# Performance work log

Hardware: AMD Instinct MI355X
Metric: run time of the kernel (lower is better)

Reference implementation:

```python
import jax, jax.numpy as jnp
import numpy as np

NX = 2048
NY = 2048
PML = 40
DT = 0.0005
DX = 10.0


def setup_inputs() -> dict:
    key = jax.random.key(0)
    k1, k2, k3, k4 = jax.random.split(key, 4)
    pad = 2 * PML
    p1 = jax.random.normal(k1, (NX + pad, NY + pad), dtype=jnp.float32)
    p2 = jax.random.normal(k2, (NX + pad, NY + pad), dtype=jnp.float32)
    varray = jax.random.uniform(k3, (NX, NY), dtype=jnp.float32)
    source_function = jax.random.normal(k4, (500,), dtype=jnp.float32)
    return {
        "p1": p1,
        "p2": p2,
        "varray": varray,
        "source_function": source_function,
        "x_s": 1024,
        "y_s": 1024,
        "t": 100,
    }


def reference(p1, p2, varray, source_function, x_s, y_s, t):
    # Extend velocity model with edge-replicated PML padding (same math as the
    # torch extend_with_pml with its 9 slice assignments).
    pml_varray = jnp.pad(varray, PML, mode="edge")
    alpha = pml_varray ** 2 * (DT ** 2)
    inv_dx2 = 1.0 / (DX * DX)
    # Second-order centered differences via shifted slices.
    dpdx = (p2[:, 9:-7] - 2.0 * p2[:, 8:-8] + p2[:, 7:-9]) * inv_dx2  # [Np, Np-16]
    dpdy = (p2[9:-7, :] - 2.0 * p2[8:-8, :] + p2[7:-9, :]) * inv_dx2  # [Np-16, Np]
    rhs = (
        2.0 * p2[8:-8, 8:-8]
        - p1[8:-8, 8:-8]
        + alpha[8:-8, 8:-8] * (dpdx[8:-8, :] + dpdy[:, 8:-8])
    )
    p = jnp.zeros_like(p1).at[8:-8, 8:-8].set(rhs)
    # Point-source injection at the (offset) source location.
    p = p.at[x_s + PML, y_s + PML].add(source_function[t] * (DT ** 2))
    res = p[PML:-PML, PML:-PML]
    return (p, res[:, 50])
```

## Files before the change

### kernel.cpp

```cpp
#include <hip/hip_runtime.h>

#define NXC   2048
#define PMLC  40
#define W     2128
#define WV    532
#define NWORK (W * WV)
#define NBLK  ((NWORK + 255) / 256)

typedef float f32x4 __attribute__((ext_vector_type(4)));

__global__ __launch_bounds__(256) void wave_step(
    const float* __restrict__ p1,
    const float* __restrict__ p2,
    const float* __restrict__ varray,
    const float* __restrict__ sf,
    const int* __restrict__ xs_p,
    const int* __restrict__ ys_p,
    const int* __restrict__ t_p,
    float* __restrict__ pout,
    float* __restrict__ col)
{
    constexpr int q = NBLK / 8, r = NBLK % 8;
    const int xcd = blockIdx.x & 7, pos = blockIdx.x >> 3;
    const int swz = (xcd < r ? xcd * (q + 1) : r * (q + 1) + (xcd - r) * q) + pos;
    const int v = (swz << 8) + (int)threadIdx.x;
    if (v >= NWORK) return;

    const int i  = v / WV;
    const int j0 = (v - i * WV) << 2;
    const size_t base = (size_t)i * W + j0;

    if (i < 8 || i >= W - 8 || j0 < 8 || j0 >= W - 8) {
        f32x4 z = {0.f, 0.f, 0.f, 0.f};
        __builtin_nontemporal_store(z, reinterpret_cast<f32x4*>(&pout[base]));
        return;
    }

    constexpr float inv_dx2 = 1.0f / (10.0f * 10.0f);
    constexpr float dt2     = 0.0005f * 0.0005f;

    const f32x4 c  = *reinterpret_cast<const f32x4*>(&p2[base]);
    const f32x4 up = *reinterpret_cast<const f32x4*>(&p2[base - W]);
    const f32x4 dn = *reinterpret_cast<const f32x4*>(&p2[base + W]);
    const f32x4 a1 = __builtin_nontemporal_load(
        reinterpret_cast<const f32x4*>(&p1[base]));
    const float lft = p2[base - 1];
    const float rgt = p2[base + 4];

    const int vi = min(max(i - PMLC, 0), NXC - 1);
    const float* __restrict__ vr = &varray[(size_t)vi * NXC];

    float vav[4];
    const int vj0 = j0 - PMLC;
    if (vj0 >= 0 && vj0 <= NXC - 4) {
        const f32x4 vv = __builtin_nontemporal_load(
            reinterpret_cast<const f32x4*>(&vr[vj0]));
        vav[0] = vv.x; vav[1] = vv.y; vav[2] = vv.z; vav[3] = vv.w;
    } else {
        #pragma unroll
        for (int k = 0; k < 4; ++k)
            vav[k] = vr[min(max(vj0 + k, 0), NXC - 1)];
    }

    const float cc[6]  = {lft, c.x, c.y, c.z, c.w, rgt};
    const float upk[4] = {up.x, up.y, up.z, up.w};
    const float dnk[4] = {dn.x, dn.y, dn.z, dn.w};
    const float a1k[4] = {a1.x, a1.y, a1.z, a1.w};
    float outk[4];

    #pragma unroll
    for (int k = 0; k < 4; ++k) {
        const float alpha = vav[k] * vav[k] * dt2;
        const float ctr   = cc[k + 1];
        const float lap   = (cc[k] + cc[k + 2] + upk[k] + dnk[k] - 4.0f * ctr) * inv_dx2;
        outk[k] = 2.0f * ctr - a1k[k] + alpha * lap;
    }

    const int xs = xs_p[0] + PMLC;
    const int ys = ys_p[0] + PMLC;
    if (i == xs) {
        const int d = ys - j0;
        if ((unsigned)d < 4u) {
            outk[d] += sf[t_p[0]] * dt2;
        }
    }

    if (j0 == 88 && (unsigned)(i - PMLC) < (unsigned)NXC) {
        col[i - PMLC] = outk[2];
    }

    f32x4 outv = {outk[0], outk[1], outk[2], outk[3]};
    __builtin_nontemporal_store(outv, reinterpret_cast<f32x4*>(&pout[base]));
}

extern "C" void kernel_launch(void* const* d_in, const int* in_sizes, int n_in,
                              void* d_out, int out_size, void* d_ws, size_t ws_size,
                              hipStream_t stream) {
    const float* p1 = (const float*)d_in[0];
    const float* p2 = (const float*)d_in[1];
    const float* va = (const float*)d_in[2];
    const float* sf = (const float*)d_in[3];
    const int* xs   = (const int*)d_in[4];
    const int* ys   = (const int*)d_in[5];
    const int* t    = (const int*)d_in[6];

    float* pout = (float*)d_out;
    float* col  = (float*)d_out + (size_t)W * W;

    wave_step<<<NBLK, 256, 0, stream>>>(p1, p2, va, sf, xs, ys, t, pout, col);
}
```

Before: 16.71 us.

## Compute two rows per thread to reuse stencil row loads

Each thread now computes a 4-wide strip in two adjacent rows. It loads four p2 rows instead of three per row, so each thread reads four rows of p2 for two outputs rather than six. The grid is halved, and the nontemporal load/store hints are replaced with ordinary accesses. This raises the number of loads in flight per thread and the register use. The L1/L2 cache may already have captured most of the row reuse, so the gain could be limited.

Result: faster. 16.29 us (-2.5%).

```diff
diff --git a/kernel.cpp b/kernel.cpp
--- a/kernel.cpp
+++ b/kernel.cpp
@@ -4,7 +4,8 @@
 #define PMLC  40
 #define W     2128
 #define WV    532
-#define NWORK (W * WV)
+#define NPAIR (W / 2)
+#define NWORK (NPAIR * WV)
 #define NBLK  ((NWORK + 255) / 256)
 
 typedef float f32x4 __attribute__((ext_vector_type(4)));
@@ -26,71 +27,88 @@
     const int v = (swz << 8) + (int)threadIdx.x;
     if (v >= NWORK) return;
 
-    const int i  = v / WV;
-    const int j0 = (v - i * WV) << 2;
-    const size_t base = (size_t)i * W + j0;
+    const int pr = v / WV;
+    const int i  = pr << 1;
+    const int j0 = (v - pr * WV) << 2;
+    const size_t base0 = (size_t)i * W + j0;
+    const size_t base1 = base0 + W;
 
     if (i < 8 || i >= W - 8 || j0 < 8 || j0 >= W - 8) {
         f32x4 z = {0.f, 0.f, 0.f, 0.f};
-        __builtin_nontemporal_store(z, reinterpret_cast<f32x4*>(&pout[base]));
+        *reinterpret_cast<f32x4*>(&pout[base0]) = z;
+        *reinterpret_cast<f32x4*>(&pout[base1]) = z;
         return;
     }
 
     constexpr float inv_dx2 = 1.0f / (10.0f * 10.0f);
     constexpr float dt2     = 0.0005f * 0.0005f;
 
-    const f32x4 c  = *reinterpret_cast<const f32x4*>(&p2[base]);
-    const f32x4 up = *reinterpret_cast<const f32x4*>(&p2[base - W]);
-    const f32x4 dn = *reinterpret_cast<const f32x4*>(&p2[base + W]);
-    const f32x4 a1 = __builtin_nontemporal_load(
-        reinterpret_cast<const f32x4*>(&p1[base]));
-    const float lft = p2[base - 1];
-    const float rgt = p2[base + 4];
+    const f32x4 rm1 = *reinterpret_cast<const f32x4*>(&p2[base0 - W]);
+    const f32x4 r0  = *reinterpret_cast<const f32x4*>(&p2[base0]);
+    const f32x4 rp1 = *reinterpret_cast<const f32x4*>(&p2[base1]);
+    const f32x4 rp2 = *reinterpret_cast<const f32x4*>(&p2[base1 + W]);
+    const f32x4 a10 = *reinterpret_cast<const f32x4*>(&p1[base0]);
+    const f32x4 a11 = *reinterpret_cast<const f32x4*>(&p1[base1]);
+    const float lft0 = p2[base0 - 1], rgt0 = p2[base0 + 4];
+    const float lft1 = p2[base1 - 1], rgt1 = p2[base1 + 4];
 
-    const int vi = min(max(i - PMLC, 0), NXC - 1);
-    const float* __restrict__ vr = &varray[(size_t)vi * NXC];
-
-    float vav[4];
+    const int vi0 = min(max(i - PMLC, 0), NXC - 1);
+    const int vi1 = min(max(i + 1 - PMLC, 0), NXC - 1);
+    const float* __restrict__ vr0 = &varray[(size_t)vi0 * NXC];
+    const float* __restrict__ vr1 = &varray[(size_t)vi1 * NXC];
+    float va0[4], va1[4];
     const int vj0 = j0 - PMLC;
     if (vj0 >= 0 && vj0 <= NXC - 4) {
-        const f32x4 vv = __builtin_nontemporal_load(
-            reinterpret_cast<const f32x4*>(&vr[vj0]));
-        vav[0] = vv.x; vav[1] = vv.y; vav[2] = vv.z; vav[3] = vv.w;
+        const f32x4 w0 = *reinterpret_cast<const f32x4*>(&vr0[vj0]);
+        const f32x4 w1 = *reinterpret_cast<const f32x4*>(&vr1[vj0]);
+        va0[0]=w0.x; va0[1]=w0.y; va0[2]=w0.z; va0[3]=w0.w;
+        va1[0]=w1.x; va1[1]=w1.y; va1[2]=w1.z; va1[3]=w1.w;
     } else {
         #pragma unroll
-        for (int k = 0; k < 4; ++k)
-            vav[k] = vr[min(max(vj0 + k, 0), NXC - 1)];
+        for (int k = 0; k < 4; ++k) {
+            const int vj = min(max(vj0 + k, 0), NXC - 1);
+            va0[k] = vr0[vj];
+            va1[k] = vr1[vj];
+        }
     }
 
-    const float cc[6]  = {lft, c.x, c.y, c.z, c.w, rgt};
-    const float upk[4] = {up.x, up.y, up.z, up.w};
-    const float dnk[4] = {dn.x, dn.y, dn.z, dn.w};
-    const float a1k[4] = {a1.x, a1.y, a1.z, a1.w};
-    float outk[4];
+    const float c0[6] = {lft0, r0.x, r0.y, r0.z, r0.w, rgt0};
+    const float c1[6] = {lft1, rp1.x, rp1.y, rp1.z, rp1.w, rgt1};
+    const float um[4] = {rm1.x, rm1.y, rm1.z, rm1.w};
+    const float dp[4] = {rp2.x, rp2.y, rp2.z, rp2.w};
+    const float a0k[4] = {a10.x, a10.y, a10.z, a10.w};
+    const float a1k[4] = {a11.x, a11.y, a11.z, a11.w};
+    float out0[4], out1[4];
 
     #pragma unroll
     for (int k = 0; k < 4; ++k) {
-        const float alpha = vav[k] * vav[k] * dt2;
-        const float ctr   = cc[k + 1];
-        const float lap   = (cc[k] + cc[k + 2] + upk[k] + dnk[k] - 4.0f * ctr) * inv_dx2;
-        outk[k] = 2.0f * ctr - a1k[k] + alpha * lap;
+        const float ctr0 = c0[k + 1];
+        const float lap0 = (c0[k] + c0[k + 2] + um[k] + c1[k + 1] - 4.0f * ctr0) * inv_dx2;
+        out0[k] = 2.0f * ctr0 - a0k[k] + va0[k] * va0[k] * dt2 * lap0;
+        const float ctr1 = c1[k + 1];
+        const float lap1 = (c1[k] + c1[k + 2] + c0[k + 1] + dp[k] - 4.0f * ctr1) * inv_dx2;
+        out1[k] = 2.0f * ctr1 - a1k[k] + va1[k] * va1[k] * dt2 * lap1;
     }
 
     const int xs = xs_p[0] + PMLC;
     const int ys = ys_p[0] + PMLC;
-    if (i == xs) {
+    if (xs - i <= 1 && xs >= i) {
         const int d = ys - j0;
         if ((unsigned)d < 4u) {
-            outk[d] += sf[t_p[0]] * dt2;
+            const float add = sf[t_p[0]] * dt2;
+            if (xs == i) out0[d] += add; else out1[d] += add;
         }
     }
 
-    if (j0 == 88 && (unsigned)(i - PMLC) < (unsigned)NXC) {
-        col[i - PMLC] = outk[2];
+    if (j0 == 88) {
+        if ((unsigned)(i - PMLC) < (unsigned)NXC)     col[i - PMLC]     = out0[2];
+        if ((unsigned)(i + 1 - PMLC) < (unsigned)NXC) col[i + 1 - PMLC] = out1[2];
     }
 
-    f32x4 outv = {outk[0], outk[1], outk[2], outk[3]};
-    __builtin_nontemporal_store(outv, reinterpret_cast<f32x4*>(&pout[base]));
+    f32x4 o0 = {out0[0], out0[1], out0[2], out0[3]};
+    f32x4 o1 = {out1[0], out1[1], out1[2], out1[3]};
+    *reinterpret_cast<f32x4*>(&pout[base0]) = o0;
+    *reinterpret_cast<f32x4*>(&pout[base1]) = o1;
 }
 
 extern "C" void kernel_launch(void* const* d_in, const int* in_sizes, int n_in,
```
